# Kernel optimization log

Hardware: AMD Instinct MI355X
Metric: run time of the kernel (lower is better)

The kernel has to match this reference:

```python
import jax, jax.numpy as jnp
import numpy as np

N, D = 8192, 128


def setup_inputs() -> dict:
    key = jax.random.key(0)
    k1, k2 = jax.random.split(key)
    z1 = jax.random.normal(k1, (N, D), dtype=jnp.float32)
    z2 = jax.random.normal(k2, (N, D), dtype=jnp.float32)
    return {"z1": z1, "z2": z2}


def reference(z1, z2):
    # logits[i, j] = -||z1_i - z2_j||^2, computed via the cdist-as-GEMM identity
    # (same math as dz = z2[None,:,:] - z1[:,None,:]; -einsum('...d,...d->...', dz, dz))
    sq1 = jnp.sum(z1 * z1, axis=-1)  # [N]
    sq2 = jnp.sum(z2 * z2, axis=-1)  # [N]
    logits = 2.0 * (z1 @ z2.T) - sq1[:, None] - sq2[None, :]  # [N, N]
    # CrossEntropyLoss with labels = arange(N): mean over rows of -log_softmax diag
    logp = jax.nn.log_softmax(logits, axis=-1)
    return -jnp.mean(jnp.diagonal(logp))
```

## Files before the change

kernel.cpp:

```cpp
#include <hip/hip_runtime.h>
#include <hip/hip_bf16.h>

typedef unsigned int   u32;
typedef unsigned short u16;

#define NN   8192
#define DD   128
#define CCH  16
#define CHUNK (NN / CCH)
#define JT   64
#define NT   (CHUNK / JT)

#define LOG2E 1.4426950408889634f
#define LN2F  0.6931471805599453f
#define BIAS  32.0f

typedef __bf16 bf16x8 __attribute__((ext_vector_type(8)));
typedef float  f32x16 __attribute__((ext_vector_type(16)));
typedef float  f32x2  __attribute__((ext_vector_type(2)));

__device__ __forceinline__ u16 f2bf(float x) {
    u32 u = __float_as_uint(x);
    u += 0x7fffu + ((u >> 16) & 1u);
    return (u16)(u >> 16);
}

__global__ __launch_bounds__(256) void prep_kernel(
    const float* __restrict__ z1, const float* __restrict__ z2,
    u32* __restrict__ b1, u32* __restrict__ b2,
    float* __restrict__ negsq2b, float* __restrict__ diag)
{
    int row  = blockIdx.x * 4 + (threadIdx.x >> 6);
    int lane = threadIdx.x & 63;
    float2 a = reinterpret_cast<const float2*>(z1)[row * 64 + lane];
    float2 b = reinterpret_cast<const float2*>(z2)[row * 64 + lane];
    b1[row * 64 + lane] = (u32)f2bf(a.x) | ((u32)f2bf(a.y) << 16);
    b2[row * 64 + lane] = (u32)f2bf(b.x) | ((u32)f2bf(b.y) << 16);
    float dot = a.x * b.x + a.y * b.y;
    float sq  = b.x * b.x + b.y * b.y;
    #pragma unroll
    for (int o = 32; o > 0; o >>= 1) {
        dot += __shfl_xor(dot, o);
        sq  += __shfl_xor(sq, o);
    }
    if (lane == 0) {
        negsq2b[row] = -sq * LOG2E - BIAS;
        diag[row]    = 2.0f * dot - sq;
    }
}

__global__ __launch_bounds__(256, 2) void score_kernel(
    const u16* __restrict__ b1, const u16* __restrict__ b2,
    const float* __restrict__ negsq2b, float* __restrict__ partS)
{
    __shared__ alignas(16) u16 tile[2][JT * DD];
    const int tid  = threadIdx.x;
    const int lane = tid & 63;
    const int wid  = tid >> 6;
    const int r    = lane & 31, hi = lane >> 5;
    const int chunk = blockIdx.x;
    const int j0    = chunk * CHUNK;
    const int i0w   = blockIdx.y * 256 + wid * 64;

    bf16x8 zf0[8], zf1[8];
    #pragma unroll
    for (int kk = 0; kk < 8; ++kk) {
        zf0[kk] = *reinterpret_cast<const bf16x8*>(b1 + (size_t)(i0w + r)      * DD + kk * 16 + hi * 8);
        zf1[kk] = *reinterpret_cast<const bf16x8*>(b1 + (size_t)(i0w + 32 + r) * DD + kk * 16 + hi * 8);
    }

    const int sl   = lane & 15;
    const int rrow = lane >> 4;

    auto stage = [&](int t, int buf) {
        #pragma unroll
        for (int u = 0; u < 4; ++u) {
            int row   = wid * 16 + u * 4 + rrow;
            int gslot = sl ^ (row & 15);
            const u16* src = b2 + (size_t)(j0 + t * JT + row) * DD + gslot * 8;
            u16* dst = &tile[buf][(wid * 16 + u * 4) * DD];
            __builtin_amdgcn_global_load_lds(
                (const __attribute__((address_space(1))) void*)src,
                (__attribute__((address_space(3))) void*)dst, 16, 0, 0);
        }
    };

    float s0 = 0.f, s1 = 0.f, s2 = 0.f, s3 = 0.f;
    const f32x2 C2v = {2.0f * LOG2E, 2.0f * LOG2E};
    const int sw = r & 15;

    int cur = 0;
    stage(0, 0);
    for (int t = 0; t < NT; ++t) {
        __syncthreads();
        if (t + 1 < NT) stage(t + 1, cur ^ 1);
        const u16* tp = tile[cur];
        #pragma unroll
        for (int jj = 0; jj < 2; ++jj) {
            const float* nqb = negsq2b + j0 + t * JT + jj * 32 + 4 * hi;
            float4 nq0 = *reinterpret_cast<const float4*>(nqb);
            float4 nq1 = *reinterpret_cast<const float4*>(nqb + 8);
            float4 nq2 = *reinterpret_cast<const float4*>(nqb + 16);
            float4 nq3 = *reinterpret_cast<const float4*>(nqb + 24);
            bf16x8 av[8];
            #pragma unroll
            for (int kk = 0; kk < 8; ++kk) {
                int off = (jj * 32 + r) * DD + (((2 * kk + hi) ^ sw) << 3);
                av[kk] = *reinterpret_cast<const bf16x8*>(tp + off);
            }
            f32x16 acc0 = {0.f}; f32x16 acc1 = {0.f};
            #pragma unroll
            for (int kk = 0; kk < 8; ++kk) {
                acc0 = __builtin_amdgcn_mfma_f32_32x32x16_bf16(av[kk], zf0[kk], acc0, 0, 0, 0);
                acc1 = __builtin_amdgcn_mfma_f32_32x32x16_bf16(av[kk], zf1[kk], acc1, 0, 0, 0);
            }
            const float nqa[16] = {nq0.x, nq0.y, nq0.z, nq0.w,
                                   nq1.x, nq1.y, nq1.z, nq1.w,
                                   nq2.x, nq2.y, nq2.z, nq2.w,
                                   nq3.x, nq3.y, nq3.z, nq3.w};
            #pragma unroll
            for (int q = 0; q < 8; ++q) {
                f32x2 n2 = {nqa[2 * q], nqa[2 * q + 1]};
                f32x2 a0 = {acc0[2 * q], acc0[2 * q + 1]};
                f32x2 t0 = a0 * C2v + n2;
                s0 += __builtin_amdgcn_exp2f(t0.x);
                s1 += __builtin_amdgcn_exp2f(t0.y);
                f32x2 a1 = {acc1[2 * q], acc1[2 * q + 1]};
                f32x2 t1 = a1 * C2v + n2;
                s2 += __builtin_amdgcn_exp2f(t1.x);
                s3 += __builtin_amdgcn_exp2f(t1.y);
            }
        }
        cur ^= 1;
    }

    float sum0 = s0 + s1, sum1 = s2 + s3;
    sum0 += __shfl_xor(sum0, 32);
    sum1 += __shfl_xor(sum1, 32);
    if (hi == 0) {
        partS[(size_t)chunk * NN + i0w + r]      = sum0;
        partS[(size_t)chunk * NN + i0w + 32 + r] = sum1;
    }
}

__global__ __launch_bounds__(256) void finalize1_kernel(
    const float* __restrict__ partS, const float* __restrict__ diag,
    float* __restrict__ blocksum)
{
    __shared__ float red[4];
    int r = blockIdx.x * 256 + threadIdx.x;
    float s = 0.f;
    #pragma unroll
    for (int c = 0; c < CCH; ++c) s += partS[(size_t)c * NN + r];
    float lse = (BIAS + __builtin_amdgcn_logf(s)) * LN2F;
    float acc = lse - diag[r];
    #pragma unroll
    for (int o = 32; o > 0; o >>= 1) acc += __shfl_xor(acc, o);
    int lane = threadIdx.x & 63, wid = threadIdx.x >> 6;
    if (lane == 0) red[wid] = acc;
    __syncthreads();
    if (threadIdx.x == 0)
        blocksum[blockIdx.x] = red[0] + red[1] + red[2] + red[3];
}

__global__ void finalize2_kernel(const float* __restrict__ blocksum, float* __restrict__ out)
{
    int lane = threadIdx.x;
    float v = (lane < 32) ? blocksum[lane] : 0.f;
    #pragma unroll
    for (int o = 32; o > 0; o >>= 1) v += __shfl_xor(v, o);
    if (lane == 0) out[0] = v * (1.0f / (float)NN);
}

extern "C" void kernel_launch(void* const* d_in, const int* in_sizes, int n_in,
                              void* d_out, int out_size, void* d_ws, size_t ws_size,
                              hipStream_t stream)
{
    const float* z1 = (const float*)d_in[0];
    const float* z2 = (const float*)d_in[1];
    char* ws = (char*)d_ws;

    const size_t bf_bytes = (size_t)NN * DD * 2;
    u32*   b1       = (u32*)ws;
    u32*   b2       = (u32*)(ws + bf_bytes);
    float* negsq2b  = (float*)(ws + 2 * bf_bytes);
    float* diag     = (float*)(ws + 2 * bf_bytes + (size_t)NN * 4);
    float* partS    = (float*)(ws + 2 * bf_bytes + (size_t)NN * 8);
    float* blocksum = (float*)(ws + 2 * bf_bytes + (size_t)NN * 8 + (size_t)CCH * NN * 4);
    float* out      = (float*)d_out;

    prep_kernel<<<NN / 4, 256, 0, stream>>>(z1, z2, b1, b2, negsq2b, diag);
    score_kernel<<<dim3(CCH, NN / 256), 256, 0, stream>>>((const u16*)b1, (const u16*)b2, negsq2b, partS);
    finalize1_kernel<<<NN / 256, 256, 0, stream>>>(partS, diag, blocksum);
    finalize2_kernel<<<1, 64, 0, stream>>>(blocksum, out);
}
```

Baseline: 35.96 us.

## Fuse finalize into score kernel via last-block reduction and triple-buffer B tiles

Removes the two finalize kernel launches by having the last 32 blocks to finish the score kernel wait on a global counter, then reduce the per-row partial sums. The final total is accumulated with a fixed-point 64-bit atomic so the result stays deterministic. The score loop also moves to triple-buffered async LDS staging with an explicit vmcnt wait in place of a full sync. It preloads negsq2b into shared memory, raises wave priority around the MFMA block, and transposes the partS layout so each row's partials are contiguous. The risks are a spin-wait that assumes all blocks become resident, plus higher LDS use that may lower occupancy.

```diff
diff --git a/kernel.cpp b/kernel.cpp
--- a/kernel.cpp
+++ b/kernel.cpp
@@ -3,6 +3,7 @@
 
 typedef unsigned int   u32;
 typedef unsigned short u16;
+typedef unsigned long long u64;
 
 #define NN   8192
 #define DD   128
@@ -10,10 +11,13 @@
 #define CHUNK (NN / CCH)
 #define JT   64
 #define NT   (CHUNK / JT)
+#define GRID (CCH * (NN / 256))
+#define NFIN 32
 
 #define LOG2E 1.4426950408889634f
 #define LN2F  0.6931471805599453f
 #define BIAS  32.0f
+#define FIXSCALE 4294967296.0
 
 typedef __bf16 bf16x8 __attribute__((ext_vector_type(8)));
 typedef float  f32x16 __attribute__((ext_vector_type(16)));
@@ -28,8 +32,9 @@
 __global__ __launch_bounds__(256) void prep_kernel(
     const float* __restrict__ z1, const float* __restrict__ z2,
     u32* __restrict__ b1, u32* __restrict__ b2,
-    float* __restrict__ negsq2b, float* __restrict__ diag)
+    float* __restrict__ negsq2b, float* __restrict__ diag, u32* __restrict__ ctrl)
 {
+    if (blockIdx.x == 0 && threadIdx.x < 4) ctrl[threadIdx.x] = 0;
     int row  = blockIdx.x * 4 + (threadIdx.x >> 6);
     int lane = threadIdx.x & 63;
     float2 a = reinterpret_cast<const float2*>(z1)[row * 64 + lane];
@@ -51,9 +56,14 @@
 
 __global__ __launch_bounds__(256, 2) void score_kernel(
     const u16* __restrict__ b1, const u16* __restrict__ b2,
-    const float* __restrict__ negsq2b, float* __restrict__ partS)
+    const float* __restrict__ negsq2b, const float* __restrict__ diag,
+    float* __restrict__ partS, u32* __restrict__ ctrl, float* __restrict__ out)
 {
-    __shared__ alignas(16) u16 tile[2][JT * DD];
+    __shared__ alignas(16) u16 tile[3][JT * DD];
+    __shared__ float nqs[CHUNK];
+    __shared__ u32 rankS;
+    __shared__ float red[4];
+
     const int tid  = threadIdx.x;
     const int lane = tid & 63;
     const int wid  = tid >> 6;
@@ -68,108 +78,129 @@
         zf0[kk] = *reinterpret_cast<const bf16x8*>(b1 + (size_t)(i0w + r)      * DD + kk * 16 + hi * 8);
         zf1[kk] = *reinterpret_cast<const bf16x8*>(b1 + (size_t)(i0w + 32 + r) * DD + kk * 16 + hi * 8);
     }
+    {
+        float2 v = reinterpret_cast<const float2*>(negsq2b + j0)[tid];
+        *reinterpret_cast<float2*>(&nqs[2 * tid]) = v;
+    }
+    __syncthreads();
 
     const int sl   = lane & 15;
     const int rrow = lane >> 4;
-
-    auto stage = [&](int t, int buf) {
+    auto stage = [&](int t, u16* dst_base) {
         #pragma unroll
         for (int u = 0; u < 4; ++u) {
             int row   = wid * 16 + u * 4 + rrow;
             int gslot = sl ^ (row & 15);
             const u16* src = b2 + (size_t)(j0 + t * JT + row) * DD + gslot * 8;
-            u16* dst = &tile[buf][(wid * 16 + u * 4) * DD];
             __builtin_amdgcn_global_load_lds(
                 (const __attribute__((address_space(1))) void*)src,
-                (__attribute__((address_space(3))) void*)dst, 16, 0, 0);
+                (__attribute__((address_space(3))) void*)(dst_base + (wid * 16 + u * 4) * DD),
+                16, 0, 0);
         }
     };
 
-    float s0 = 0.f, s1 = 0.f, s2 = 0.f, s3 = 0.f;
-    const f32x2 C2v = {2.0f * LOG2E, 2.0f * LOG2E};
+    u16 *pa = tile[0], *pb = tile[1], *pc = tile[2];
+    stage(0, pa);
+    stage(1, pb);
+
+    const f32x2 c2 = {2.0f * LOG2E, 2.0f * LOG2E};
     const int sw = r & 15;
-
-    int cur = 0;
-    stage(0, 0);
+    f32x2 sA0 = {0.f, 0.f}, sA1 = {0.f, 0.f}, sB0 = {0.f, 0.f}, sB1 = {0.f, 0.f};
+
     for (int t = 0; t < NT; ++t) {
-        __syncthreads();
-        if (t + 1 < NT) stage(t + 1, cur ^ 1);
-        const u16* tp = tile[cur];
+        asm volatile("s_waitcnt vmcnt(4)" ::: "memory");
+        __builtin_amdgcn_s_barrier();
+        __builtin_amdgcn_sched_barrier(0);
+        if (t + 2 < NT) stage(t + 2, pc);
+        const u16* tp = pa;
         #pragma unroll
         for (int jj = 0; jj < 2; ++jj) {
-            const float* nqb = negsq2b + j0 + t * JT + jj * 32 + 4 * hi;
-            float4 nq0 = *reinterpret_cast<const float4*>(nqb);
-            float4 nq1 = *reinterpret_cast<const float4*>(nqb + 8);
-            float4 nq2 = *reinterpret_cast<const float4*>(nqb + 16);
-            float4 nq3 = *reinterpret_cast<const float4*>(nqb + 24);
+            const float* nql = nqs + t * JT + jj * 32 + 4 * hi;
+            float4 nq0 = *reinterpret_cast<const float4*>(nql);
+            float4 nq1 = *reinterpret_cast<const float4*>(nql + 8);
+            float4 nq2 = *reinterpret_cast<const float4*>(nql + 16);
+            float4 nq3 = *reinterpret_cast<const float4*>(nql + 24);
             bf16x8 av[8];
             #pragma unroll
-            for (int kk = 0; kk < 8; ++kk) {
-                int off = (jj * 32 + r) * DD + (((2 * kk + hi) ^ sw) << 3);
-                av[kk] = *reinterpret_cast<const bf16x8*>(tp + off);
-            }
+            for (int kk = 0; kk < 8; ++kk)
+                av[kk] = *reinterpret_cast<const bf16x8*>(tp + (jj * 32 + r) * DD + (((2 * kk + hi) ^ sw) << 3));
             f32x16 acc0 = {0.f}; f32x16 acc1 = {0.f};
+            __builtin_amdgcn_s_setprio(1);
             #pragma unroll
             for (int kk = 0; kk < 8; ++kk) {
                 acc0 = __builtin_amdgcn_mfma_f32_32x32x16_bf16(av[kk], zf0[kk], acc0, 0, 0, 0);
                 acc1 = __builtin_amdgcn_mfma_f32_32x32x16_bf16(av[kk], zf1[kk], acc1, 0, 0, 0);
             }
-            const float nqa[16] = {nq0.x, nq0.y, nq0.z, nq0.w,
-                                   nq1.x, nq1.y, nq1.z, nq1.w,
-                                   nq2.x, nq2.y, nq2.z, nq2.w,
-                                   nq3.x, nq3.y, nq3.z, nq3.w};
+            __builtin_amdgcn_s_setprio(0);
+            const float4 nqm[4] = {nq0, nq1, nq2, nq3};
             #pragma unroll
-            for (int q = 0; q < 8; ++q) {
-                f32x2 n2 = {nqa[2 * q], nqa[2 * q + 1]};
-                f32x2 a0 = {acc0[2 * q], acc0[2 * q + 1]};
-                f32x2 t0 = a0 * C2v + n2;
-                s0 += __builtin_amdgcn_exp2f(t0.x);
-                s1 += __builtin_amdgcn_exp2f(t0.y);
-                f32x2 a1 = {acc1[2 * q], acc1[2 * q + 1]};
-                f32x2 t1 = a1 * C2v + n2;
-                s2 += __builtin_amdgcn_exp2f(t1.x);
-                s3 += __builtin_amdgcn_exp2f(t1.y);
+            for (int m = 0; m < 4; ++m) {
+                f32x2 n01 = {nqm[m].x, nqm[m].y}, n23 = {nqm[m].z, nqm[m].w};
+                f32x2 a01 = {acc0[4*m], acc0[4*m+1]}, a23 = {acc0[4*m+2], acc0[4*m+3]};
+                f32x2 t01 = a01 * c2 + n01, t23 = a23 * c2 + n23;
+                f32x2 e01 = {__builtin_amdgcn_exp2f(t01.x), __builtin_amdgcn_exp2f(t01.y)};
+                f32x2 e23 = {__builtin_amdgcn_exp2f(t23.x), __builtin_amdgcn_exp2f(t23.y)};
+                sA0 += e01; sA1 += e23;
+                f32x2 b01 = {acc1[4*m], acc1[4*m+1]}, b23 = {acc1[4*m+2], acc1[4*m+3]};
+                f32x2 u01 = b01 * c2 + n01, u23 = b23 * c2 + n23;
+                f32x2 f01 = {__builtin_amdgcn_exp2f(u01.x), __builtin_amdgcn_exp2f(u01.y)};
+                f32x2 f23 = {__builtin_amdgcn_exp2f(u23.x), __builtin_amdgcn_exp2f(u23.y)};
+                sB0 += f01; sB1 += f23;
             }
         }
-        cur ^= 1;
-    }
-
-    float sum0 = s0 + s1, sum1 = s2 + s3;
+        u16* tmp = pa; pa = pb; pb = pc; pc = tmp;
+    }
+
+    float sum0 = (sA0.x + sA0.y) + (sA1.x + sA1.y);
+    float sum1 = (sB0.x + sB0.y) + (sB1.x + sB1.y);
     sum0 += __shfl_xor(sum0, 32);
     sum1 += __shfl_xor(sum1, 32);
     if (hi == 0) {
-        partS[(size_t)chunk * NN + i0w + r]      = sum0;
-        partS[(size_t)chunk * NN + i0w + 32 + r] = sum1;
-    }
-}
-
-__global__ __launch_bounds__(256) void finalize1_kernel(
-    const float* __restrict__ partS, const float* __restrict__ diag,
-    float* __restrict__ blocksum)
-{
-    __shared__ float red[4];
-    int r = blockIdx.x * 256 + threadIdx.x;
-    float s = 0.f;
-    #pragma unroll
-    for (int c = 0; c < CCH; ++c) s += partS[(size_t)c * NN + r];
-    float lse = (BIAS + __builtin_amdgcn_logf(s)) * LN2F;
-    float acc = lse - diag[r];
-    #pragma unroll
-    for (int o = 32; o > 0; o >>= 1) acc += __shfl_xor(acc, o);
-    int lane = threadIdx.x & 63, wid = threadIdx.x >> 6;
-    if (lane == 0) red[wid] = acc;
+        partS[(size_t)(i0w + r)      * CCH + chunk] = sum0;
+        partS[(size_t)(i0w + 32 + r) * CCH + chunk] = sum1;
+    }
+
+    u32* counter  = ctrl;
+    u32* counter2 = ctrl + 1;
+    u64* acc64    = (u64*)(ctrl + 2);
+
+    __threadfence();
     __syncthreads();
-    if (threadIdx.x == 0)
-        blocksum[blockIdx.x] = red[0] + red[1] + red[2] + red[3];
-}
-
-__global__ void finalize2_kernel(const float* __restrict__ blocksum, float* __restrict__ out)
-{
-    int lane = threadIdx.x;
-    float v = (lane < 32) ? blocksum[lane] : 0.f;
-    #pragma unroll
-    for (int o = 32; o > 0; o >>= 1) v += __shfl_xor(v, o);
-    if (lane == 0) out[0] = v * (1.0f / (float)NN);
+    if (tid == 0) rankS = atomicAdd(counter, 1u);
+    __syncthreads();
+    const u32 rank = rankS;
+    if (rank >= GRID - NFIN) {
+        if (tid == 0) {
+            while (__hip_atomic_load(counter, __ATOMIC_RELAXED, __HIP_MEMORY_SCOPE_AGENT) < GRID)
+                __builtin_amdgcn_s_sleep(2);
+        }
+        __syncthreads();
+        __threadfence();
+        const int slice = (int)rank - (GRID - NFIN);
+        const int row   = slice * 256 + tid;
+        const float4* pr = reinterpret_cast<const float4*>(partS + (size_t)row * CCH);
+        float4 q0 = pr[0], q1 = pr[1], q2 = pr[2], q3 = pr[3];
+        float s = ((q0.x + q0.y) + (q0.z + q0.w)) + ((q1.x + q1.y) + (q1.z + q1.w))
+                + ((q2.x + q2.y) + (q2.z + q2.w)) + ((q3.x + q3.y) + (q3.z + q3.w));
+        float lse = (BIAS + __builtin_amdgcn_logf(s)) * LN2F;
+        float a = lse - diag[row];
+        #pragma unroll
+        for (int o = 32; o > 0; o >>= 1) a += __shfl_xor(a, o);
+        if (lane == 0) red[wid] = a;
+        __syncthreads();
+        if (tid == 0) {
+            float tot = (red[0] + red[1]) + (red[2] + red[3]);
+            long long v = (long long)llrint((double)tot * FIXSCALE);
+            atomicAdd(acc64, (u64)v);
+            __threadfence();
+            u32 o2 = atomicAdd(counter2, 1u);
+            if (o2 == NFIN - 1) {
+                __threadfence();
+                long long total = (long long)__hip_atomic_load(acc64, __ATOMIC_RELAXED, __HIP_MEMORY_SCOPE_AGENT);
+                out[0] = (float)((double)total / FIXSCALE / (double)NN);
+            }
+        }
+    }
 }
 
 extern "C" void kernel_launch(void* const* d_in, const int* in_sizes, int n_in,
@@ -181,16 +212,15 @@
     char* ws = (char*)d_ws;
 
     const size_t bf_bytes = (size_t)NN * DD * 2;
-    u32*   b1       = (u32*)ws;
-    u32*   b2       = (u32*)(ws + bf_bytes);
-    float* negsq2b  = (float*)(ws + 2 * bf_bytes);
-    float* diag     = (float*)(ws + 2 * bf_bytes + (size_t)NN * 4);
-    float* partS    = (float*)(ws + 2 * bf_bytes + (size_t)NN * 8);
-    float* blocksum = (float*)(ws + 2 * bf_bytes + (size_t)NN * 8 + (size_t)CCH * NN * 4);
-    float* out      = (float*)d_out;
-
-    prep_kernel<<<NN / 4, 256, 0, stream>>>(z1, z2, b1, b2, negsq2b, diag);
-    score_kernel<<<dim3(CCH, NN / 256), 256, 0, stream>>>((const u16*)b1, (const u16*)b2, negsq2b, partS);
-    finalize1_kernel<<<NN / 256, 256, 0, stream>>>(partS, diag, blocksum);
-    finalize2_kernel<<<1, 64, 0, stream>>>(blocksum, out);
-}
+    u32*   b1      = (u32*)ws;
+    u32*   b2      = (u32*)(ws + bf_bytes);
+    float* negsq2b = (float*)(ws + 2 * bf_bytes);
+    float* diag    = (float*)(ws + 2 * bf_bytes + (size_t)NN * 4);
+    float* partS   = (float*)(ws + 2 * bf_bytes + (size_t)NN * 8);
+    u32*   ctrl    = (u32*)(ws + 2 * bf_bytes + (size_t)NN * 8 + (size_t)NN * CCH * 4);
+    float* out     = (float*)d_out;
+
+    prep_kernel<<<NN / 4, 256, 0, stream>>>(z1, z2, b1, b2, negsq2b, diag, ctrl);
+    score_kernel<<<dim3(CCH, NN / 256), 256, 0, stream>>>(
+        (const u16*)b1, (const u16*)b2, negsq2b, diag, partS, ctrl, out);
+}
```

New measurement: 94.71 us. 2.63x slower.
